# Performance work log

Hardware: AMD Instinct MI355X
Metric: run time of the kernel (lower is better)

Reference implementation:

```python
import jax, jax.numpy as jnp
import numpy as np

ALPHA = 0.95
B, T, IN, HID, CTX, OUT = 64, 512, 256, 512, 256, 128
HORIZON = 1


def _scrn_layer(x, Wx, bx, Uc, Vh):
    # x: [B, T, D_in]; Wx: [CTX, D_in]; bx: [CTX]; Uc: [HID, CTX]; Vh: [HID, HID]
    # Input projection is time-parallel; only the recurrence is sequential.
    xp = jnp.einsum('btd,cd->btc', x, Wx) + bx  # [B, T, CTX]
    h0 = jnp.zeros((x.shape[0], Vh.shape[0]), dtype=x.dtype)
    c0 = jnp.zeros((x.shape[0], Wx.shape[0]), dtype=x.dtype)

    def step(carry, xp_t):
        h, c = carry
        c = (1.0 - ALPHA) * c + ALPHA * xp_t
        h = jnp.tanh(jnp.dot(c, Uc.T) + jnp.dot(h, Vh.T))
        return (h, c), h

    (_, _), hs = jax.lax.scan(step, (h0, c0), jnp.swapaxes(xp, 0, 1))
    return jnp.swapaxes(hs, 0, 1)  # [B, T, HID]


def setup_inputs() -> dict:
    key = jax.random.key(0)
    ks = jax.random.split(key, 12)

    def lin(k, fan_in, shape):
        bound = 1.0 / np.sqrt(fan_in)
        return jax.random.uniform(k, shape, jnp.float32, -bound, bound)

    return {
        'x': jax.random.normal(ks[0], (B, T, IN), jnp.float32),
        'Wx0': lin(ks[1], IN, (CTX, IN)),
        'bx0': lin(ks[2], IN, (CTX,)),
        'Uc0': lin(ks[3], CTX, (HID, CTX)),
        'Vh0': lin(ks[4], HID, (HID, HID)),
        'Wx1': lin(ks[5], HID, (CTX, HID)),
        'bx1': lin(ks[6], HID, (CTX,)),
        'Uc1': lin(ks[7], CTX, (HID, CTX)),
        'Vh1': lin(ks[8], HID, (HID, HID)),
        'fc_w': lin(ks[9], HID, (OUT, HID)),
        'fc_b': lin(ks[10], HID, (OUT,)),
    }


def reference(x, Wx0, bx0, Uc0, Vh0, Wx1, bx1, Uc1, Vh1, fc_w, fc_b):
    out = _scrn_layer(x, Wx0, bx0, Uc0, Vh0)
    out = _scrn_layer(out, Wx1, bx1, Uc1, Vh1)
    out = out[:, -HORIZON:, :]  # [B, HORIZON, HID]
    return jnp.einsum('bth,oh->bto', out, fc_w) + fc_b  # [B, HORIZON, OUT]
```

## Files before the change

kernel.cpp:

```cpp
#include <hip/hip_runtime.h>


typedef _Float16 f16;
typedef _Float16 f16x8 __attribute__((ext_vector_type(8)));
typedef _Float16 f16x2 __attribute__((ext_vector_type(2)));
typedef float f32x4 __attribute__((ext_vector_type(4)));
typedef unsigned short u16;
typedef unsigned int u32;
typedef unsigned short u16x8 __attribute__((ext_vector_type(8)));
typedef unsigned long long u64;

#define DEV __device__ __forceinline__

constexpr int Tt = 512, HIDq = 512;

DEV float bf2f(u16 u) { unsigned v = ((unsigned)u) << 16; float f; __builtin_memcpy(&f, &v, 4); return f; }
DEV u16 f2bf(float f) { unsigned u; __builtin_memcpy(&u, &f, 4); u = (u + 0x7fffu + ((u >> 16) & 1u)) >> 16; return (u16)u; }
DEV float fast_tanh(float x) {
  x = fminf(30.f, fmaxf(-30.f, x));
  float e = exp2f(x * 2.885390081777927f);
  return (e - 1.f) / (e + 1.f);
}
DEV u64 al64(const u64* p) { return __hip_atomic_load(p, __ATOMIC_RELAXED, __HIP_MEMORY_SCOPE_AGENT); }
DEV u32 al32(const u32* p) { return __hip_atomic_load(p, __ATOMIC_RELAXED, __HIP_MEMORY_SCOPE_AGENT); }
DEV void as32(u32* p, u32 v) { __hip_atomic_store(p, v, __ATOMIC_RELAXED, __HIP_MEMORY_SCOPE_AGENT); }

__global__ void k_probe(const u16* __restrict__ w, int* __restrict__ dmode) {
  __shared__ int s;
  if (threadIdx.x == 0) s = 0;
  __syncthreads();
  int found = 0;
  for (int i = threadIdx.x; i < 8192; i += 256) {
    float v = bf2f(w[i]);
    if (fabsf(v) > 0.5f) found = 1;
  }
  if (found) atomicOr(&s, 1);
  __syncthreads();
  if (threadIdx.x == 0) *dmode = s;
}

__global__ void k_cvt(const void* __restrict__ src, f16* __restrict__ dst, int n8,
                      const int* __restrict__ dmode) {
  int i = blockIdx.x * 256 + threadIdx.x;
  if (i >= n8) return;
  f16x8 o;
  if (*dmode) {
    const float4* s = (const float4*)src;
    float4 a = s[2*i], b = s[2*i+1];
    o[0]=(f16)a.x; o[1]=(f16)a.y; o[2]=(f16)a.z; o[3]=(f16)a.w;
    o[4]=(f16)b.x; o[5]=(f16)b.y; o[6]=(f16)b.z; o[7]=(f16)b.w;
  } else {
    u16x8 v = ((const u16x8*)src)[i];
#pragma unroll
    for (int j = 0; j < 8; ++j) o[j] = (f16)bf2f(v[j]);
  }
  ((f16x8*)dst)[i] = o;
}

__global__ void k_zero(u16* __restrict__ out) {
  out[blockIdx.x * 256 + threadIdx.x] = 0;
}

__global__ __launch_bounds__(256) void k_tr(const f16* __restrict__ src, f16* __restrict__ dst,
                                            int R, int cshift) {
  int idx = blockIdx.x * 256 + threadIdx.x;
  int r = idx >> cshift, c = idx & ((1 << cshift) - 1);
  dst[c * R + r] = src[idx];
}

__global__ __launch_bounds__(512) void k_bias(const f16* __restrict__ Uc, const f16* __restrict__ bx,
                                              f16* __restrict__ out) {
  int j = threadIdx.x;
  float a = 0.f;
  for (int c = 0; c < 256; ++c) a += (float)Uc[j * 256 + c] * (float)bx[c];
  out[j] = (f16)a;
}

__global__ __launch_bounds__(128) void k_ema(const f16* __restrict__ xp, f16* __restrict__ c) {
  int b = blockIdx.x >> 3, chunk = blockIdx.x & 7;
  int t0 = chunk * 64;
  int ch = threadIdx.x;
  const f16x2* src = (const f16x2*)(xp + (size_t)b * Tt * 256) + ch;
  f16x2* dst = (f16x2*)(c + (size_t)b * Tt * 256) + ch;
  float c0 = 0.f, c1 = 0.f;
  int ts = (t0 >= 16) ? t0 - 16 : 0;
  for (int tt = ts; tt < t0 + 64; ++tt) {
    f16x2 v = src[(size_t)tt * 128];
    c0 = 0.05f * c0 + 0.95f * (float)v.x;
    c1 = 0.05f * c1 + 0.95f * (float)v.y;
    if (tt >= t0) { f16x2 o; o.x = (f16)c0; o.y = (f16)c1; dst[(size_t)tt * 128] = o; }
  }
}

template<bool HAS_BIAS, bool TD>
__global__ __launch_bounds__(256) void k_gemm(const f16* __restrict__ A, const f16* __restrict__ Bm,
                                              const f16* __restrict__ bias, f16* __restrict__ C,
                                              int M, int N, int K) {
  __shared__ f16 As[128][40];
  __shared__ f16 Bs[128][40];
  const int tid = threadIdx.x, lane = tid & 63, wv = tid >> 6;
  const int l15 = lane & 15, q = lane >> 4;
  const int wm = wv >> 1, wn = wv & 1;
  const int m0 = blockIdx.y * 128, n0 = blockIdx.x * 128;
  const int srow = tid >> 1, sseg = tid & 1;
  f32x4 acc[4][4] = {};
  const f16* ga = A  + (size_t)(m0 + srow) * K + sseg * 16;
  const f16* gb = Bm + (size_t)(n0 + srow) * K + sseg * 16;
  for (int k0 = 0; k0 < K; k0 += 32) {
    f16x8 a0 = *(const f16x8*)(ga + k0);
    f16x8 a1 = *(const f16x8*)(ga + k0 + 8);
    f16x8 b0 = *(const f16x8*)(gb + k0);
    f16x8 b1 = *(const f16x8*)(gb + k0 + 8);
    __syncthreads();
    *(f16x8*)&As[srow][sseg*16]     = a0;
    *(f16x8*)&As[srow][sseg*16 + 8] = a1;
    *(f16x8*)&Bs[srow][sseg*16]     = b0;
    *(f16x8*)&Bs[srow][sseg*16 + 8] = b1;
    __syncthreads();
    f16x8 af[4], bf[4];
#pragma unroll
    for (int i = 0; i < 4; ++i) af[i] = *(const f16x8*)&As[wm*64 + i*16 + l15][q*8];
#pragma unroll
    for (int i = 0; i < 4; ++i) bf[i] = *(const f16x8*)&Bs[wn*64 + i*16 + l15][q*8];
#pragma unroll
    for (int i = 0; i < 4; ++i)
#pragma unroll
      for (int j = 0; j < 4; ++j)
        acc[i][j] = __builtin_amdgcn_mfma_f32_16x16x32_f16(af[i], bf[j], acc[i][j], 0, 0, 0);
  }
#pragma unroll
  for (int j = 0; j < 4; ++j) {
    int col = n0 + wn*64 + j*16 + l15;
    float bv = HAS_BIAS ? (float)bias[col] : 0.f;
#pragma unroll
    for (int i = 0; i < 4; ++i)
#pragma unroll
      for (int r = 0; r < 4; ++r) {
        int row = m0 + wm*64 + i*16 + q*4 + r;
        size_t orow = TD ? (size_t)((row & 511) * 64 + (row >> 9)) : (size_t)row;
        C[orow * N + col] = (f16)(acc[i][j][r] + bv);
      }
  }
}

__global__ __launch_bounds__(512, 2) void k_mega(const f16* __restrict__ Vh0,
                                                 const f16* __restrict__ Vh1,
                                                 const f16* __restrict__ W2,
                                                 const f16* __restrict__ b2,
                                                 const f16* __restrict__ d1,
                                                 u32* __restrict__ ring,
                                                 u32* __restrict__ d2r,
                                                 u32* __restrict__ hb2,
                                                 u32* __restrict__ prog) {
  __shared__ f16 hL[2][16][520];
  const int bb = blockIdx.x;
  const int tid = threadIdx.x, w = tid >> 6, lane = tid & 63;
  const int l15 = lane & 15, q = lane >> 4;

  if (bb < 8) {
    const int hf = bb & 1, g = bb >> 1;
    const int colbase = 256*hf + 32*w;
    f16x8 Bf[2][16];
#pragma unroll
    for (int j = 0; j < 2; ++j)
#pragma unroll
      for (int kk = 0; kk < 16; ++kk)
        Bf[j][kk] = *(const f16x8*)&Vh0[(size_t)(colbase + 16*j + l15) * HIDq + kk*32 + q*8];
    for (int i = tid; i < 1024; i += 512) {
      int r = i >> 6, c = (i & 63) * 8;
      f16x8 z = {};
      *(f16x8*)&hL[0][r][c] = z;
    }
    float dv[2][4];
#pragma unroll
    for (int j = 0; j < 2; ++j)
#pragma unroll
      for (int r = 0; r < 4; ++r)
        dv[j][r] = (float)d1[(size_t)(16*g + q*4 + r) * HIDq + colbase + 16*j + l15];
    __syncthreads();
    const int irow = tid >> 5, ic8 = (tid & 31) * 8;
    const int pcol = 256*(hf ^ 1) + ic8;

    for (int t = 0; t < Tt; ++t) {
      const int rb = t & 1, wb = rb ^ 1;
      u32* rslot = ring + (size_t)(t & 255) * 32768;
      f32x4 a00 = {}, a01 = {}, a10 = {}, a11 = {};
#pragma unroll
      for (int kk = 0; kk < 16; ++kk) {
        f16x8 a = *(const f16x8*)&hL[rb][l15][kk*32 + q*8];
        if (kk & 1) {
          a01 = __builtin_amdgcn_mfma_f32_16x16x32_f16(a, Bf[0][kk], a01, 0, 0, 0);
          a11 = __builtin_amdgcn_mfma_f32_16x16x32_f16(a, Bf[1][kk], a11, 0, 0, 0);
        } else {
          a00 = __builtin_amdgcn_mfma_f32_16x16x32_f16(a, Bf[0][kk], a00, 0, 0, 0);
          a10 = __builtin_amdgcn_mfma_f32_16x16x32_f16(a, Bf[1][kk], a10, 0, 0, 0);
        }
      }
      const u32 tagw = (u32)(t + 1) << 16;
      u16 hbits[2][4];
#pragma unroll
      for (int j = 0; j < 2; ++j) {
        f32x4 s = j ? (a10 + a11) : (a00 + a01);
#pragma unroll
        for (int r = 0; r < 4; ++r) {
          float z = s[r] + dv[j][r];
          union { f16 h; u16 u; } cv; cv.h = (f16)fast_tanh(z);
          hbits[j][r] = cv.u;
          as32(&rslot[(size_t)(16*g + q*4 + r) * HIDq + colbase + 16*j + l15],
               tagw | (u32)cv.u);
        }
      }
#pragma unroll
      for (int j = 0; j < 2; ++j)
#pragma unroll
        for (int r = 0; r < 4; ++r) {
          union { u16 u; f16 h; } cv; cv.u = hbits[j][r];
          hL[wb][q*4 + r][colbase + 16*j + l15] = cv.h;
        }
      if (t < Tt - 1) {
#pragma unroll
        for (int j = 0; j < 2; ++j)
#pragma unroll
          for (int r = 0; r < 4; ++r)
            dv[j][r] = (float)d1[((size_t)(t+1)*64 + 16*g + q*4 + r) * HIDq + colbase + 16*j + l15];
      }
      {
        const u64* pp = (const u64*)(rslot + (size_t)(16*g + irow) * HIDq) + (pcol >> 1);
        u64 v[4];
#pragma unroll
        for (int jj = 0; jj < 4; ++jj) v[jj] = al64(pp + jj);
        for (;;) {
          u32 bad = 0;
#pragma unroll
          for (int jj = 0; jj < 4; ++jj)
            bad |= ((u32)v[jj] ^ tagw) | ((u32)(v[jj] >> 32) ^ tagw);
          if ((bad & 0xFFFF0000u) == 0) break;
          __builtin_amdgcn_s_sleep(1);
#pragma unroll
          for (int jj = 0; jj < 4; ++jj) v[jj] = al64(pp + jj);
        }
        union { u32 wd[4]; f16x8 vv; } fr;
#pragma unroll
        for (int jj = 0; jj < 4; ++jj)
          fr.wd[jj] = __builtin_amdgcn_perm((u32)(v[jj] >> 32), (u32)v[jj], 0x05040100u);
        *(f16x8*)&hL[wb][irow][pcol] = fr.vv;
      }
      __syncthreads();
    }

  } else if (bb < 16) {
    const int eb = bb - 8, hf = eb & 1, g = eb >> 1;
    const int colbase = 256*hf + 32*w;
    f16x8 Bf[2][16];
#pragma unroll
    for (int j = 0; j < 2; ++j)
#pragma unroll
      for (int kk = 0; kk < 16; ++kk)
        Bf[j][kk] = *(const f16x8*)&W2[(size_t)(colbase + 16*j + l15) * HIDq + kk*32 + q*8];
    float bv[2] = { (float)b2[colbase + l15], (float)b2[colbase + 16 + l15] };
    float ed[2][4] = {};
    const int irow = tid >> 5, icol = (tid & 31) * 16;
    int eprog_c = 0;

    for (int t = 0; t < Tt; ++t) {
      if (tid == 0 && t >= 129 && eprog_c < t - 128) {
        for (;;) {
          eprog_c = (int)al32(&prog[eb]);
          if (eprog_c >= t - 128) break;
          __builtin_amdgcn_s_sleep(1);
        }
      }
      const u32 tagw = (u32)(t + 1) << 16;
      {
        const u64* pp = (const u64*)(ring + (size_t)(t & 255) * 32768
                          + (size_t)(16*g + irow) * HIDq) + (icol >> 1);
        u64 v[8];
#pragma unroll
        for (int jj = 0; jj < 8; ++jj) v[jj] = al64(pp + jj);
        for (;;) {
          u32 bad = 0;
#pragma unroll
          for (int jj = 0; jj < 8; ++jj)
            bad |= ((u32)v[jj] ^ tagw) | ((u32)(v[jj] >> 32) ^ tagw);
          if ((bad & 0xFFFF0000u) == 0) break;
          __builtin_amdgcn_s_sleep(1);
#pragma unroll
          for (int jj = 0; jj < 8; ++jj) v[jj] = al64(pp + jj);
        }
        union { u32 wd[8]; f16x8 vv[2]; } fr;
#pragma unroll
        for (int jj = 0; jj < 8; ++jj)
          fr.wd[jj] = __builtin_amdgcn_perm((u32)(v[jj] >> 32), (u32)v[jj], 0x05040100u);
        *(f16x8*)&hL[t & 1][irow][icol]     = fr.vv[0];
        *(f16x8*)&hL[t & 1][irow][icol + 8] = fr.vv[1];
      }
      __syncthreads();
      f32x4 a00 = {}, a01 = {}, a10 = {}, a11 = {};
#pragma unroll
      for (int kk = 0; kk < 16; ++kk) {
        f16x8 a = *(const f16x8*)&hL[t & 1][l15][kk*32 + q*8];
        if (kk & 1) {
          a01 = __builtin_amdgcn_mfma_f32_16x16x32_f16(a, Bf[0][kk], a01, 0, 0, 0);
          a11 = __builtin_amdgcn_mfma_f32_16x16x32_f16(a, Bf[1][kk], a11, 0, 0, 0);
        } else {
          a00 = __builtin_amdgcn_mfma_f32_16x16x32_f16(a, Bf[0][kk], a00, 0, 0, 0);
          a10 = __builtin_amdgcn_mfma_f32_16x16x32_f16(a, Bf[1][kk], a10, 0, 0, 0);
        }
      }
      u32* dslot = d2r + (size_t)(t & 127) * 32768;
#pragma unroll
      for (int j = 0; j < 2; ++j) {
        f32x4 s = j ? (a10 + a11) : (a00 + a01);
#pragma unroll
        for (int r = 0; r < 4; ++r) {
          ed[j][r] = 0.05f * ed[j][r] + 0.95f * (s[r] + bv[j]);
          union { f16 h; u16 u; } cv; cv.h = (f16)ed[j][r];
          as32(&dslot[(size_t)(16*g + q*4 + r) * HIDq + colbase + 16*j + l15],
               tagw | (u32)cv.u);
        }
      }
    }

  } else {
    const int sb = bb - 16, hf = sb & 1, g = sb >> 1;
    const int colbase = 256*hf + 32*w;
    f16x8 Bf[2][16];
#pragma unroll
    for (int j = 0; j < 2; ++j)
#pragma unroll
      for (int kk = 0; kk < 16; ++kk)
        Bf[j][kk] = *(const f16x8*)&Vh1[(size_t)(colbase + 16*j + l15) * HIDq + kk*32 + q*8];
    for (int i = tid; i < 1024; i += 512) {
      int r = i >> 6, c = (i & 63) * 8;
      f16x8 z = {};
      *(f16x8*)&hL[0][r][c] = z;
    }
    float dv[2][4];
    {
      const u32 tag2 = 1u << 16;
      const u32* dp = d2r + (size_t)(16*g + q*4) * HIDq + colbase + l15;
      u32 vv[8];
      for (;;) {
#pragma unroll
        for (int i = 0; i < 8; ++i) vv[i] = al32(dp + (size_t)(i & 3) * HIDq + 16*(i >> 2));
        u32 bad = 0;
#pragma unroll
        for (int i = 0; i < 8; ++i) bad |= vv[i] ^ tag2;
        if ((bad & 0xFFFF0000u) == 0) break;
        __builtin_amdgcn_s_sleep(1);
      }
#pragma unroll
      for (int j = 0; j < 2; ++j)
#pragma unroll
        for (int r = 0; r < 4; ++r) {
          union { u16 u; f16 h; } cv; cv.u = (u16)vv[j*4 + r];
          dv[j][r] = (float)cv.h;
        }
    }
    __syncthreads();
    const int irow = tid >> 5, ic8 = (tid & 31) * 8;
    const int pcol = 256*(hf ^ 1) + ic8;

    for (int t = 0; t < Tt; ++t) {
      const int rb = t & 1, wb = rb ^ 1, slot = t & 1;
      if (tid == 0 && t > 0) as32(&prog[sb], (u32)t);
      f32x4 a00 = {}, a01 = {}, a10 = {}, a11 = {};
#pragma unroll
      for (int kk = 0; kk < 16; ++kk) {
        f16x8 a = *(const f16x8*)&hL[rb][l15][kk*32 + q*8];
        if (kk & 1) {
          a01 = __builtin_amdgcn_mfma_f32_16x16x32_f16(a, Bf[0][kk], a01, 0, 0, 0);
          a11 = __builtin_amdgcn_mfma_f32_16x16x32_f16(a, Bf[1][kk], a11, 0, 0, 0);
        } else {
          a00 = __builtin_amdgcn_mfma_f32_16x16x32_f16(a, Bf[0][kk], a00, 0, 0, 0);
          a10 = __builtin_amdgcn_mfma_f32_16x16x32_f16(a, Bf[1][kk], a10, 0, 0, 0);
        }
      }
      const u32 tagw = (u32)(t + 1) << 16;
      u16 hbits[2][4];
#pragma unroll
      for (int j = 0; j < 2; ++j) {
        f32x4 s = j ? (a10 + a11) : (a00 + a01);
#pragma unroll
        for (int r = 0; r < 4; ++r) {
          float z = s[r] + dv[j][r];
          union { f16 h; u16 u; } cv; cv.h = (f16)fast_tanh(z);
          hbits[j][r] = cv.u;
          as32(&hb2[(size_t)(slot*64 + 16*g + q*4 + r) * HIDq + colbase + 16*j + l15],
               tagw | (u32)cv.u);
        }
      }
#pragma unroll
      for (int j = 0; j < 2; ++j)
#pragma unroll
        for (int r = 0; r < 4; ++r) {
          union { u16 u; f16 h; } cv; cv.u = hbits[j][r];
          hL[wb][q*4 + r][colbase + 16*j + l15] = cv.h;
        }

      {
        const bool have_d = (t < Tt - 1);
        const u32 tag2 = (u32)(t + 2) << 16;
        const u32* dp = d2r + (size_t)((t + 1) & 127) * 32768
                      + (size_t)(16*g + q*4) * HIDq + colbase + l15;
        const u64* pp = (const u64*)&hb2[(size_t)(slot*64 + 16*g + irow) * HIDq] + (pcol >> 1);
        u32 vv[8];
        u64 v[4];
        if (have_d) {
#pragma unroll
          for (int i = 0; i < 8; ++i) vv[i] = al32(dp + (size_t)(i & 3) * HIDq + 16*(i >> 2));
        }
#pragma unroll
        for (int jj = 0; jj < 4; ++jj) v[jj] = al64(pp + jj);
        for (;;) {
          u32 badp = 0;
#pragma unroll
          for (int jj = 0; jj < 4; ++jj)
            badp |= ((u32)v[jj] ^ tagw) | ((u32)(v[jj] >> 32) ^ tagw);
          badp &= 0xFFFF0000u;
          u32 badd = 0;
          if (have_d) {
#pragma unroll
            for (int i = 0; i < 8; ++i) badd |= vv[i] ^ tag2;
            badd &= 0xFFFF0000u;
          }
          if (!(badp | badd)) break;
          __builtin_amdgcn_s_sleep(1);
          if (badp) {
#pragma unroll
            for (int jj = 0; jj < 4; ++jj) v[jj] = al64(pp + jj);
          }
          if (badd) {
#pragma unroll
            for (int i = 0; i < 8; ++i) vv[i] = al32(dp + (size_t)(i & 3) * HIDq + 16*(i >> 2));
          }
        }
        if (have_d) {
#pragma unroll
          for (int j = 0; j < 2; ++j)
#pragma unroll
            for (int r = 0; r < 4; ++r) {
              union { u16 u; f16 h; } cv; cv.u = (u16)vv[j*4 + r];
              dv[j][r] = (float)cv.h;
            }
        }
        union { u32 wd[4]; f16x8 vr; } fr;
#pragma unroll
        for (int jj = 0; jj < 4; ++jj)
          fr.wd[jj] = __builtin_amdgcn_perm((u32)(v[jj] >> 32), (u32)v[jj], 0x05040100u);
        *(f16x8*)&hL[wb][irow][pcol] = fr.vr;
      }
      __syncthreads();
    }
  }
}

__global__ __launch_bounds__(64) void k_final(const u32* __restrict__ h, const f16* __restrict__ fw,
                                              const f16* __restrict__ fb, void* __restrict__ outv,
                                              const int* __restrict__ dmode) {
  __shared__ f16 hA[16][520];
  __shared__ f16 Bw[16][520];
  const int mb = blockIdx.x & 3, nb = blockIdx.x >> 2;
  const int lane = threadIdx.x, l15 = lane & 15, q = lane >> 4;
  for (int i = lane; i < 16 * 128; i += 64) {
    int r = i >> 7, c = (i & 127) * 4;
    const u64* p = (const u64*)&h[(size_t)(mb*16 + r) * 512 + c];
    u64 v0 = al64(p), v1 = al64(p + 1);
    *(u32*)&hA[r][c]     = __builtin_amdgcn_perm((u32)(v0 >> 32), (u32)v0, 0x05040100u);
    *(u32*)&hA[r][c + 2] = __builtin_amdgcn_perm((u32)(v1 >> 32), (u32)v1, 0x05040100u);
  }
  for (int i = lane; i < 16 * 64; i += 64) {
    int r = i >> 6, c = (i & 63) * 8;
    *(f16x8*)&Bw[r][c] = *(const f16x8*)&fw[(size_t)(nb*16 + r) * 512 + c];
  }
  __syncthreads();
  f32x4 acc = {};
#pragma unroll
  for (int kk = 0; kk < 16; ++kk) {
    f16x8 a = *(const f16x8*)&hA[l15][kk*32 + q*8];
    f16x8 b = *(const f16x8*)&Bw[l15][kk*32 + q*8];
    acc = __builtin_amdgcn_mfma_f32_16x16x32_f16(a, b, acc, 0, 0, 0);
  }
  float bv = (float)fb[nb*16 + l15];
  int md = *dmode;
#pragma unroll
  for (int r = 0; r < 4; ++r) {
    int idx = (mb*16 + q*4 + r) * 128 + nb*16 + l15;
    float val = acc[r] + bv;
    if (md) ((float*)outv)[idx] = val;
    else    ((u16*)outv)[idx]   = f2bf(val);
  }
}

extern "C" void kernel_launch(void* const* d_in, const int* in_sizes, int n_in,
                              void* d_out, int out_size, void* d_ws, size_t ws_size,
                              hipStream_t stream) {
  if (ws_size < 88080384ull) {
    k_zero<<<32, 256, 0, stream>>>((u16*)d_out);
    return;
  }
  char* ws = (char*)d_ws;
  u32* hb2   = (u32*)(ws + 0);
  u32* prog  = (u32*)(ws + 262144);
  int* dmode = (int*)(ws + 262208);
  f16* Wx0f = (f16*)(ws + 262656);
  f16* Uc0f = (f16*)(ws + 393728);
  f16* Vh0f = (f16*)(ws + 655872);
  f16* Wx1f = (f16*)(ws + 1180160);
  f16* Uc1f = (f16*)(ws + 1442304);
  f16* Vh1f = (f16*)(ws + 1704448);
  f16* fcwf = (f16*)(ws + 2228736);
  f16* bx0f = (f16*)(ws + 2359808);
  f16* bx1f = (f16*)(ws + 2360320);
  f16* fcbf = (f16*)(ws + 2360832);
  f16* Wx1T = (f16*)(ws + 2361344);
  f16* W2f  = (f16*)(ws + 2623488);
  f16* b2f  = (f16*)(ws + 3147776);
  f16* x16  = (f16*)(ws + 4194304);
  u32* ring = (u32*)(ws + 4194304);
  f16* xp1  = (f16*)(ws + 20971520);
  f16* cb1  = (f16*)(ws + 37748736);
  u32* d2r  = (u32*)(ws + 37748736);
  f16* d1   = (f16*)(ws + 54525952);

  k_probe<<<1, 256, 0, stream>>>((const u16*)d_in[1], dmode);
  auto cvt = [&](const void* s, f16* d, int n) {
    int n8 = n / 8;
    k_cvt<<<dim3((n8 + 255) / 256), dim3(256), 0, stream>>>(s, d, n8, dmode);
  };
  cvt(d_in[0],  x16,  8388608);
  cvt(d_in[1],  Wx0f, 65536);
  cvt(d_in[2],  bx0f, 256);
  cvt(d_in[3],  Uc0f, 131072);
  cvt(d_in[4],  Vh0f, 262144);
  cvt(d_in[5],  Wx1f, 131072);
  cvt(d_in[6],  bx1f, 256);
  cvt(d_in[7],  Uc1f, 131072);
  cvt(d_in[8],  Vh1f, 262144);
  cvt(d_in[9],  fcwf, 65536);
  cvt(d_in[10], fcbf, 128);

  k_tr<<<512, 256, 0, stream>>>(Wx1f, Wx1T, 256, 9);
  k_bias<<<1, 512, 0, stream>>>(Uc1f, bx1f, b2f);
  k_gemm<false, false><<<dim3(4, 4), 256, 0, stream>>>(Uc1f, Wx1T, nullptr, W2f, 512, 512, 256);

  k_gemm<true , false><<<dim3(2, 256), 256, 0, stream>>>(x16, Wx0f, bx0f, xp1, 32768, 256, 256);
  k_ema<<<512, 128, 0, stream>>>(xp1, cb1);
  hipMemsetAsync(ws + 4194304, 0, 33554432, stream);
  k_gemm<false, true ><<<dim3(4, 256), 256, 0, stream>>>(cb1, Uc0f, nullptr, d1, 32768, 512, 256);
  hipMemsetAsync(ws + 37748736, 0, 16777216, stream);
  hipMemsetAsync(ws, 0, 262176, stream);

  k_mega<<<24, 512, 0, stream>>>(Vh0f, Vh1f, W2f, b2f, d1, ring, d2r, hb2, prog);

  k_final<<<32, 64, 0, stream>>>(hb2 + 64 * 512, fcwf, fcbf, d_out, dmode);
}
```

Before: 1.901 ms.

## Shrink inter-block ring buffers with backpressure flow control between stages

The layer-0 ring shrinks from 256 to 32 slots and the d2 ring from 128 to 32 slots. This keeps the working set of the persistent megakernel's inter-block communication small enough to stay cache-resident, and cuts the memsets that clear them. To stay correct with fewer slots, a new eprog counter lets layer-0 producer blocks wait for the consumer blocks to catch up, and the consumer's own backpressure window is tightened. The cost is extra spin-waiting and tighter coupling between stages, which can introduce stalls in the pipeline.

```diff
diff --git a/kernel.cpp b/kernel.cpp
--- a/kernel.cpp
+++ b/kernel.cpp
@@ -13,6 +13,8 @@
 #define DEV __device__ __forceinline__
 
 constexpr int Tt = 512, HIDq = 512;
+constexpr int RS = 32;
+constexpr int DSd = 32;
 
 DEV float bf2f(u16 u) { unsigned v = ((unsigned)u) << 16; float f; __builtin_memcpy(&f, &v, 4); return f; }
 DEV u16 f2bf(float f) { unsigned u; __builtin_memcpy(&u, &f, 4); u = (u + 0x7fffu + ((u >> 16) & 1u)) >> 16; return (u16)u; }
@@ -151,7 +153,8 @@
                                                  u32* __restrict__ ring,
                                                  u32* __restrict__ d2r,
                                                  u32* __restrict__ hb2,
-                                                 u32* __restrict__ prog) {
+                                                 u32* __restrict__ prog,
+                                                 u32* __restrict__ eprog) {
   __shared__ f16 hL[2][16][520];
   const int bb = blockIdx.x;
   const int tid = threadIdx.x, w = tid >> 6, lane = tid & 63;
@@ -180,10 +183,11 @@
     __syncthreads();
     const int irow = tid >> 5, ic8 = (tid & 31) * 8;
     const int pcol = 256*(hf ^ 1) + ic8;
+    int eprog_c = 0;
 
     for (int t = 0; t < Tt; ++t) {
       const int rb = t & 1, wb = rb ^ 1;
-      u32* rslot = ring + (size_t)(t & 255) * 32768;
+      u32* rslot = ring + (size_t)(t & (RS - 1)) * 32768;
       f32x4 a00 = {}, a01 = {}, a10 = {}, a11 = {};
 #pragma unroll
       for (int kk = 0; kk < 16; ++kk) {
@@ -224,6 +228,16 @@
           for (int r = 0; r < 4; ++r)
             dv[j][r] = (float)d1[((size_t)(t+1)*64 + 16*g + q*4 + r) * HIDq + colbase + 16*j + l15];
       }
+      if (tid == 0 && eprog_c < t - 30) {
+        const u64* ep = (const u64*)&eprog[2 * g];
+        for (;;) {
+          u64 e2 = al64(ep);
+          int lo = (int)(u32)e2, hi = (int)(u32)(e2 >> 32);
+          eprog_c = lo < hi ? lo : hi;
+          if (eprog_c >= t - 30) break;
+          __builtin_amdgcn_s_sleep(1);
+        }
+      }
       {
         const u64* pp = (const u64*)(rslot + (size_t)(16*g + irow) * HIDq) + (pcol >> 1);
         u64 v[4];
@@ -260,19 +274,22 @@
     float bv[2] = { (float)b2[colbase + l15], (float)b2[colbase + 16 + l15] };
     float ed[2][4] = {};
     const int irow = tid >> 5, icol = (tid & 31) * 16;
-    int eprog_c = 0;
+    int sprog_c = 0;
 
     for (int t = 0; t < Tt; ++t) {
-      if (tid == 0 && t >= 129 && eprog_c < t - 128) {
-        for (;;) {
-          eprog_c = (int)al32(&prog[eb]);
-          if (eprog_c >= t - 128) break;
-          __builtin_amdgcn_s_sleep(1);
+      if (tid == 0) {
+        if (t > 0) as32(&eprog[eb], (u32)t);
+        if (sprog_c < t - 32) {
+          for (;;) {
+            sprog_c = (int)al32(&prog[eb]);
+            if (sprog_c >= t - 32) break;
+            __builtin_amdgcn_s_sleep(1);
+          }
         }
       }
       const u32 tagw = (u32)(t + 1) << 16;
       {
-        const u64* pp = (const u64*)(ring + (size_t)(t & 255) * 32768
+        const u64* pp = (const u64*)(ring + (size_t)(t & (RS - 1)) * 32768
                           + (size_t)(16*g + irow) * HIDq) + (icol >> 1);
         u64 v[8];
 #pragma unroll
@@ -307,7 +324,7 @@
           a10 = __builtin_amdgcn_mfma_f32_16x16x32_f16(a, Bf[1][kk], a10, 0, 0, 0);
         }
       }
-      u32* dslot = d2r + (size_t)(t & 127) * 32768;
+      u32* dslot = d2r + (size_t)(t & (DSd - 1)) * 32768;
 #pragma unroll
       for (int j = 0; j < 2; ++j) {
         f32x4 s = j ? (a10 + a11) : (a00 + a01);
@@ -401,7 +418,7 @@
       {
         const bool have_d = (t < Tt - 1);
         const u32 tag2 = (u32)(t + 2) << 16;
-        const u32* dp = d2r + (size_t)((t + 1) & 127) * 32768
+        const u32* dp = d2r + (size_t)((t + 1) & (DSd - 1)) * 32768
                       + (size_t)(16*g + q*4) * HIDq + colbase + l15;
         const u64* pp = (const u64*)&hb2[(size_t)(slot*64 + 16*g + irow) * HIDq] + (pcol >> 1);
         u32 vv[8];
@@ -502,6 +519,7 @@
   char* ws = (char*)d_ws;
   u32* hb2   = (u32*)(ws + 0);
   u32* prog  = (u32*)(ws + 262144);
+  u32* eprog = (u32*)(ws + 262176);
   int* dmode = (int*)(ws + 262208);
   f16* Wx0f = (f16*)(ws + 262656);
   f16* Uc0f = (f16*)(ws + 393728);
@@ -546,12 +564,12 @@
 
   k_gemm<true , false><<<dim3(2, 256), 256, 0, stream>>>(x16, Wx0f, bx0f, xp1, 32768, 256, 256);
   k_ema<<<512, 128, 0, stream>>>(xp1, cb1);
-  hipMemsetAsync(ws + 4194304, 0, 33554432, stream);
+  hipMemsetAsync(ws + 4194304, 0, 4194304, stream);
   k_gemm<false, true ><<<dim3(4, 256), 256, 0, stream>>>(cb1, Uc0f, nullptr, d1, 32768, 512, 256);
-  hipMemsetAsync(ws + 37748736, 0, 16777216, stream);
-  hipMemsetAsync(ws, 0, 262176, stream);
-
-  k_mega<<<24, 512, 0, stream>>>(Vh0f, Vh1f, W2f, b2f, d1, ring, d2r, hb2, prog);
+  hipMemsetAsync(ws + 37748736, 0, 4194304, stream);
+  hipMemsetAsync(ws, 0, 262208, stream);
+
+  k_mega<<<24, 512, 0, stream>>>(Vh0f, Vh1f, W2f, b2f, d1, ring, d2r, hb2, prog, eprog);
 
   k_final<<<32, 64, 0, stream>>>(hb2 + 64 * 512, fcwf, fcbf, d_out, dmode);
 }
```

Result: faster. 1.827 ms, median of 2 (-3.9%).

## Fuse layer-2 input projection into layer-1 recurrence blocks, drop intermediate ring

Applied to the files above, without the earlier changes.

The separate middle group of 8 blocks, which read layer-1 h from a 256-slot ring and computed the W2 projection plus the EMA, is removed. The layer-1 blocks now compute that projection for the previous step directly from their shared-memory h and write tagged values into a smaller 32-slot d2 ring. The layer-1 h exchange uses a 2-slot buffer, and memsets shrink accordingly. This removes a global round-trip and one pipeline stage, and launches 16 blocks instead of 24. In exchange it adds MFMA work and uncached W2 loads from global memory to the critical recurrence path, plus a throttle that waits on layer-2 progress.

```diff
diff --git a/kernel.cpp b/kernel.cpp
--- a/kernel.cpp
+++ b/kernel.cpp
@@ -13,6 +13,7 @@
 #define DEV __device__ __forceinline__
 
 constexpr int Tt = 512, HIDq = 512;
+constexpr int DSd = 32;
 
 DEV float bf2f(u16 u) { unsigned v = ((unsigned)u) << 16; float f; __builtin_memcpy(&f, &v, 4); return f; }
 DEV u16 f2bf(float f) { unsigned u; __builtin_memcpy(&u, &f, 4); u = (u + 0x7fffu + ((u >> 16) & 1u)) >> 16; return (u16)u; }
@@ -143,13 +144,13 @@
   }
 }
 
-__global__ __launch_bounds__(512, 2) void k_mega(const f16* __restrict__ Vh0,
+__global__ __launch_bounds__(512, 1) void k_mega(const f16* __restrict__ Vh0,
                                                  const f16* __restrict__ Vh1,
                                                  const f16* __restrict__ W2,
                                                  const f16* __restrict__ b2,
                                                  const f16* __restrict__ d1,
-                                                 u32* __restrict__ ring,
                                                  u32* __restrict__ d2r,
+                                                 u32* __restrict__ hb1,
                                                  u32* __restrict__ hb2,
                                                  u32* __restrict__ prog) {
   __shared__ f16 hL[2][16][520];
@@ -166,6 +167,8 @@
 #pragma unroll
       for (int kk = 0; kk < 16; ++kk)
         Bf[j][kk] = *(const f16x8*)&Vh0[(size_t)(colbase + 16*j + l15) * HIDq + kk*32 + q*8];
+    float bve[2] = { (float)b2[colbase + l15], (float)b2[colbase + 16 + l15] };
+    float ed[2][4] = {};
     for (int i = tid; i < 1024; i += 512) {
       int r = i >> 6, c = (i & 63) * 8;
       f16x8 z = {};
@@ -180,10 +183,10 @@
     __syncthreads();
     const int irow = tid >> 5, ic8 = (tid & 31) * 8;
     const int pcol = 256*(hf ^ 1) + ic8;
+    int prog_c = 0;
 
     for (int t = 0; t < Tt; ++t) {
-      const int rb = t & 1, wb = rb ^ 1;
-      u32* rslot = ring + (size_t)(t & 255) * 32768;
+      const int rb = t & 1, wb = rb ^ 1, slot = t & 1;
       f32x4 a00 = {}, a01 = {}, a10 = {}, a11 = {};
 #pragma unroll
       for (int kk = 0; kk < 16; ++kk) {
@@ -206,7 +209,7 @@
           float z = s[r] + dv[j][r];
           union { f16 h; u16 u; } cv; cv.h = (f16)fast_tanh(z);
           hbits[j][r] = cv.u;
-          as32(&rslot[(size_t)(16*g + q*4 + r) * HIDq + colbase + 16*j + l15],
+          as32(&hb1[(size_t)slot * 32768 + (size_t)(16*g + q*4 + r) * HIDq + colbase + 16*j + l15],
                tagw | (u32)cv.u);
         }
       }
@@ -217,6 +220,35 @@
           union { u16 u; f16 h; } cv; cv.u = hbits[j][r];
           hL[wb][q*4 + r][colbase + 16*j + l15] = cv.h;
         }
+      if (t > 0) {
+        f32x4 e00 = {}, e01 = {}, e10 = {}, e11 = {};
+#pragma unroll
+        for (int kk = 0; kk < 16; ++kk) {
+          f16x8 a  = *(const f16x8*)&hL[rb][l15][kk*32 + q*8];
+          f16x8 w0 = *(const f16x8*)&W2[(size_t)(colbase + l15) * HIDq + kk*32 + q*8];
+          f16x8 w1 = *(const f16x8*)&W2[(size_t)(colbase + 16 + l15) * HIDq + kk*32 + q*8];
+          if (kk & 1) {
+            e01 = __builtin_amdgcn_mfma_f32_16x16x32_f16(a, w0, e01, 0, 0, 0);
+            e11 = __builtin_amdgcn_mfma_f32_16x16x32_f16(a, w1, e11, 0, 0, 0);
+          } else {
+            e00 = __builtin_amdgcn_mfma_f32_16x16x32_f16(a, w0, e00, 0, 0, 0);
+            e10 = __builtin_amdgcn_mfma_f32_16x16x32_f16(a, w1, e10, 0, 0, 0);
+          }
+        }
+        const u32 tagd = (u32)t << 16;
+        u32* dslot = d2r + (size_t)((t - 1) & (DSd - 1)) * 32768;
+#pragma unroll
+        for (int j = 0; j < 2; ++j) {
+          f32x4 se = j ? (e10 + e11) : (e00 + e01);
+#pragma unroll
+          for (int r = 0; r < 4; ++r) {
+            ed[j][r] = 0.05f * ed[j][r] + 0.95f * (se[r] + bve[j]);
+            union { f16 h; u16 u; } cv; cv.h = (f16)ed[j][r];
+            as32(&dslot[(size_t)(16*g + q*4 + r) * HIDq + colbase + 16*j + l15],
+                 tagd | (u32)cv.u);
+          }
+        }
+      }
       if (t < Tt - 1) {
 #pragma unroll
         for (int j = 0; j < 2; ++j)
@@ -225,7 +257,8 @@
             dv[j][r] = (float)d1[((size_t)(t+1)*64 + 16*g + q*4 + r) * HIDq + colbase + 16*j + l15];
       }
       {
-        const u64* pp = (const u64*)(rslot + (size_t)(16*g + irow) * HIDq) + (pcol >> 1);
+        const u64* pp = (const u64*)(hb1 + (size_t)slot * 32768 + (size_t)(16*g + irow) * HIDq)
+                      + (pcol >> 1);
         u64 v[4];
 #pragma unroll
         for (int jj = 0; jj < 4; ++jj) v[jj] = al64(pp + jj);
@@ -245,84 +278,55 @@
           fr.wd[jj] = __builtin_amdgcn_perm((u32)(v[jj] >> 32), (u32)v[jj], 0x05040100u);
         *(f16x8*)&hL[wb][irow][pcol] = fr.vv;
       }
+      if (tid == 0 && prog_c < t - 32) {
+        for (;;) {
+          prog_c = (int)al32(&prog[2*g + hf]);
+          if (prog_c >= t - 32) break;
+          __builtin_amdgcn_s_sleep(1);
+        }
+      }
       __syncthreads();
     }
-
-  } else if (bb < 16) {
-    const int eb = bb - 8, hf = eb & 1, g = eb >> 1;
-    const int colbase = 256*hf + 32*w;
-    f16x8 Bf[2][16];
-#pragma unroll
-    for (int j = 0; j < 2; ++j)
-#pragma unroll
-      for (int kk = 0; kk < 16; ++kk)
-        Bf[j][kk] = *(const f16x8*)&W2[(size_t)(colbase + 16*j + l15) * HIDq + kk*32 + q*8];
-    float bv[2] = { (float)b2[colbase + l15], (float)b2[colbase + 16 + l15] };
-    float ed[2][4] = {};
-    const int irow = tid >> 5, icol = (tid & 31) * 16;
-    int eprog_c = 0;
-
-    for (int t = 0; t < Tt; ++t) {
-      if (tid == 0 && t >= 129 && eprog_c < t - 128) {
-        for (;;) {
-          eprog_c = (int)al32(&prog[eb]);
-          if (eprog_c >= t - 128) break;
-          __builtin_amdgcn_s_sleep(1);
-        }
-      }
-      const u32 tagw = (u32)(t + 1) << 16;
-      {
-        const u64* pp = (const u64*)(ring + (size_t)(t & 255) * 32768
-                          + (size_t)(16*g + irow) * HIDq) + (icol >> 1);
-        u64 v[8];
-#pragma unroll
-        for (int jj = 0; jj < 8; ++jj) v[jj] = al64(pp + jj);
-        for (;;) {
-          u32 bad = 0;
-#pragma unroll
-          for (int jj = 0; jj < 8; ++jj)
-            bad |= ((u32)v[jj] ^ tagw) | ((u32)(v[jj] >> 32) ^ tagw);
-          if ((bad & 0xFFFF0000u) == 0) break;
-          __builtin_amdgcn_s_sleep(1);
-#pragma unroll
-          for (int jj = 0; jj < 8; ++jj) v[jj] = al64(pp + jj);
-        }
-        union { u32 wd[8]; f16x8 vv[2]; } fr;
-#pragma unroll
-        for (int jj = 0; jj < 8; ++jj)
-          fr.wd[jj] = __builtin_amdgcn_perm((u32)(v[jj] >> 32), (u32)v[jj], 0x05040100u);
-        *(f16x8*)&hL[t & 1][irow][icol]     = fr.vv[0];
-        *(f16x8*)&hL[t & 1][irow][icol + 8] = fr.vv[1];
-      }
-      __syncthreads();
-      f32x4 a00 = {}, a01 = {}, a10 = {}, a11 = {};
+    if (tid == 0 && prog_c < 479) {
+      for (;;) {
+        prog_c = (int)al32(&prog[2*g + hf]);
+        if (prog_c >= 479) break;
+        __builtin_amdgcn_s_sleep(1);
+      }
+    }
+    __syncthreads();
+    {
+      f32x4 e00 = {}, e01 = {}, e10 = {}, e11 = {};
 #pragma unroll
       for (int kk = 0; kk < 16; ++kk) {
-        f16x8 a = *(const f16x8*)&hL[t & 1][l15][kk*32 + q*8];
+        f16x8 a  = *(const f16x8*)&hL[0][l15][kk*32 + q*8];
+        f16x8 w0 = *(const f16x8*)&W2[(size_t)(colbase + l15) * HIDq + kk*32 + q*8];
+        f16x8 w1 = *(const f16x8*)&W2[(size_t)(colbase + 16 + l15) * HIDq + kk*32 + q*8];
         if (kk & 1) {
-          a01 = __builtin_amdgcn_mfma_f32_16x16x32_f16(a, Bf[0][kk], a01, 0, 0, 0);
-          a11 = __builtin_amdgcn_mfma_f32_16x16x32_f16(a, Bf[1][kk], a11, 0, 0, 0);
+          e01 = __builtin_amdgcn_mfma_f32_16x16x32_f16(a, w0, e01, 0, 0, 0);
+          e11 = __builtin_amdgcn_mfma_f32_16x16x32_f16(a, w1, e11, 0, 0, 0);
         } else {
-          a00 = __builtin_amdgcn_mfma_f32_16x16x32_f16(a, Bf[0][kk], a00, 0, 0, 0);
-          a10 = __builtin_amdgcn_mfma_f32_16x16x32_f16(a, Bf[1][kk], a10, 0, 0, 0);
-        }
-      }
-      u32* dslot = d2r + (size_t)(t & 127) * 32768;
+          e00 = __builtin_amdgcn_mfma_f32_16x16x32_f16(a, w0, e00, 0, 0, 0);
+          e10 = __builtin_amdgcn_mfma_f32_16x16x32_f16(a, w1, e10, 0, 0, 0);
+        }
+      }
+      const u32 tagd = (u32)Tt << 16;
+      u32* dslot = d2r + (size_t)((Tt - 1) & (DSd - 1)) * 32768;
 #pragma unroll
       for (int j = 0; j < 2; ++j) {
-        f32x4 s = j ? (a10 + a11) : (a00 + a01);
+        f32x4 se = j ? (e10 + e11) : (e00 + e01);
 #pragma unroll
         for (int r = 0; r < 4; ++r) {
-          ed[j][r] = 0.05f * ed[j][r] + 0.95f * (s[r] + bv[j]);
+          ed[j][r] = 0.05f * ed[j][r] + 0.95f * (se[r] + bve[j]);
           union { f16 h; u16 u; } cv; cv.h = (f16)ed[j][r];
           as32(&dslot[(size_t)(16*g + q*4 + r) * HIDq + colbase + 16*j + l15],
-               tagw | (u32)cv.u);
+               tagd | (u32)cv.u);
         }
       }
     }
 
   } else {
-    const int sb = bb - 16, hf = sb & 1, g = sb >> 1;
+    const int sb = bb - 8, hf = sb & 1, g = sb >> 1;
     const int colbase = 256*hf + 32*w;
     f16x8 Bf[2][16];
 #pragma unroll
@@ -401,7 +405,7 @@
       {
         const bool have_d = (t < Tt - 1);
         const u32 tag2 = (u32)(t + 2) << 16;
-        const u32* dp = d2r + (size_t)((t + 1) & 127) * 32768
+        const u32* dp = d2r + (size_t)((t + 1) & (DSd - 1)) * 32768
                       + (size_t)(16*g + q*4) * HIDq + colbase + l15;
         const u64* pp = (const u64*)&hb2[(size_t)(slot*64 + 16*g + irow) * HIDq] + (pcol >> 1);
         u32 vv[8];
@@ -501,28 +505,29 @@
   }
   char* ws = (char*)d_ws;
   u32* hb2   = (u32*)(ws + 0);
-  u32* prog  = (u32*)(ws + 262144);
-  int* dmode = (int*)(ws + 262208);
-  f16* Wx0f = (f16*)(ws + 262656);
-  f16* Uc0f = (f16*)(ws + 393728);
-  f16* Vh0f = (f16*)(ws + 655872);
-  f16* Wx1f = (f16*)(ws + 1180160);
-  f16* Uc1f = (f16*)(ws + 1442304);
-  f16* Vh1f = (f16*)(ws + 1704448);
-  f16* fcwf = (f16*)(ws + 2228736);
-  f16* bx0f = (f16*)(ws + 2359808);
-  f16* bx1f = (f16*)(ws + 2360320);
-  f16* fcbf = (f16*)(ws + 2360832);
-  f16* Wx1T = (f16*)(ws + 2361344);
-  f16* W2f  = (f16*)(ws + 2623488);
-  f16* b2f  = (f16*)(ws + 3147776);
+  u32* hb1   = (u32*)(ws + 262144);
+  u32* prog  = (u32*)(ws + 524288);
+  int* dmode = (int*)(ws + 524352);
+  f16* Wx0f = (f16*)(ws + 1048576);
+  f16* Uc0f = (f16*)(ws + 1179648);
+  f16* Vh0f = (f16*)(ws + 1441792);
+  f16* Wx1f = (f16*)(ws + 1966080);
+  f16* Uc1f = (f16*)(ws + 2228224);
+  f16* Vh1f = (f16*)(ws + 2490368);
+  f16* fcwf = (f16*)(ws + 3014656);
+  f16* bx0f = (f16*)(ws + 3145728);
+  f16* bx1f = (f16*)(ws + 3146240);
+  f16* fcbf = (f16*)(ws + 3146752);
+  f16* Wx1T = (f16*)(ws + 3147776);
+  f16* W2f  = (f16*)(ws + 3409920);
+  f16* b2f  = (f16*)(ws + 3934208);
   f16* x16  = (f16*)(ws + 4194304);
-  u32* ring = (u32*)(ws + 4194304);
+  u32* d2r  = (u32*)(ws + 4194304);
   f16* xp1  = (f16*)(ws + 20971520);
   f16* cb1  = (f16*)(ws + 37748736);
-  u32* d2r  = (u32*)(ws + 37748736);
   f16* d1   = (f16*)(ws + 54525952);
 
+  hipMemsetAsync(ws, 0, 524352, stream);
   k_probe<<<1, 256, 0, stream>>>((const u16*)d_in[1], dmode);
   auto cvt = [&](const void* s, f16* d, int n) {
     int n8 = n / 8;
@@ -546,12 +551,10 @@
 
   k_gemm<true , false><<<dim3(2, 256), 256, 0, stream>>>(x16, Wx0f, bx0f, xp1, 32768, 256, 256);
   k_ema<<<512, 128, 0, stream>>>(xp1, cb1);
-  hipMemsetAsync(ws + 4194304, 0, 33554432, stream);
+  hipMemsetAsync(ws + 4194304, 0, 4194304, stream);
   k_gemm<false, true ><<<dim3(4, 256), 256, 0, stream>>>(cb1, Uc0f, nullptr, d1, 32768, 512, 256);
-  hipMemsetAsync(ws + 37748736, 0, 16777216, stream);
-  hipMemsetAsync(ws, 0, 262176, stream);
-
-  k_mega<<<24, 512, 0, stream>>>(Vh0f, Vh1f, W2f, b2f, d1, ring, d2r, hb2, prog);
+
+  k_mega<<<16, 512, 0, stream>>>(Vh0f, Vh1f, W2f, b2f, d1, d2r, hb1, hb2, prog);
 
   k_final<<<32, 64, 0, stream>>>(hb2 + 64 * 512, fcwf, fcbf, d_out, dmode);
 }
```

Result: slower. 5.279 ms (+177.7%).
